# Optimization experiments

Measured on AMD Instinct MI355X. Metric: run time of the kernel, lower is better.

## Reference

```python
import jax, jax.numpy as jnp
import numpy as np

EMBED = 1024
HEADS = 16
HEAD_DIM = EMBED // HEADS


def setup_inputs() -> dict:
    key = jax.random.key(0)
    ks = jax.random.split(key, 11)
    B, S, E = 4, 2048, EMBED
    scale = 1.0 / np.sqrt(E)
    inp = {
        "Q": jax.random.normal(ks[0], (B, S, E), jnp.float32),
        "K": jax.random.normal(ks[1], (B, S, E), jnp.float32),
        "V": jax.random.normal(ks[2], (B, S, E), jnp.float32),
        "Wq": jax.random.normal(ks[3], (E, E), jnp.float32) * scale,
        "Wk": jax.random.normal(ks[4], (E, E), jnp.float32) * scale,
        "Wv": jax.random.normal(ks[5], (E, E), jnp.float32) * scale,
        "Wo": jax.random.normal(ks[6], (E, E), jnp.float32) * scale,
        "bq": jax.random.normal(ks[7], (E,), jnp.float32) * 0.01,
        "bk": jax.random.normal(ks[8], (E,), jnp.float32) * 0.01,
        "bv": jax.random.normal(ks[9], (E,), jnp.float32) * 0.01,
        "bo": jax.random.normal(ks[10], (E,), jnp.float32) * 0.01,
    }
    return inp


def reference(Q, K, V, Wq, Wk, Wv, Wo, bq, bk, bv, bo):
    B, S, E = Q.shape
    H, Dh = HEADS, HEAD_DIM
    # linear projections (torch Linear: x @ W.T + b)
    q = (Q @ Wq.T + bq).reshape(B, S, H, Dh).transpose(0, 2, 1, 3)  # [B,H,S,Dh]
    k = (K @ Wk.T + bk).reshape(B, S, H, Dh).transpose(0, 2, 1, 3)
    v = (V @ Wv.T + bv).reshape(B, S, H, Dh).transpose(0, 2, 1, 3)
    # scores [B,H,S,S]
    A = jnp.einsum('bhqd,bhkd->bhqk', q, k) / np.sqrt(Dh).astype(np.float32)
    # causal mask (mask=True)
    causal = jnp.tril(jnp.ones((S, S), dtype=bool))
    A = jnp.where(causal, A, -jnp.inf)
    w = jax.nn.softmax(A, axis=-1)
    out = jnp.einsum('bhqk,bhkd->bhqd', w, v)  # [B,H,S,Dh]
    out = out.transpose(0, 2, 1, 3).reshape(B, S, E)
    return out @ Wo.T + bo
```

## Files before the change

### kernel.cpp

```cpp
#include <hip/hip_runtime.h>
#include <hip/hip_bf16.h>
#include <hip/hip_fp16.h>

#define E_DIM 1024
#define N_HEADS 16
#define DH 64
#define BATCH 4
#define SEQ 2048
#define MROWS (BATCH * SEQ)
#define NQT 16

using half8 = __attribute__((ext_vector_type(8))) _Float16;
using half4v = __attribute__((ext_vector_type(4))) _Float16;
using fp16x2 = __attribute__((ext_vector_type(2))) __fp16;
using f32x4 = __attribute__((ext_vector_type(4))) float;

#define LOG2E 1.44269504088896340736f

__device__ inline half8 ld8(const _Float16* p) { return *(const half8*)p; }

__device__ inline uint32_t lds_off(const void* p) {
    return (uint32_t)(uintptr_t)(const __attribute__((address_space(3))) char*)p;
}

__device__ inline float exp2fast(float x) {
    float r;
    asm("v_exp_f32 %0, %1" : "=v"(r) : "v"(x));
    return r;
}

#define GLOAD_LDS(SRC, DST) \
    __builtin_amdgcn_global_load_lds( \
        (const __attribute__((address_space(1))) unsigned int*)(SRC), \
        (__attribute__((address_space(3))) unsigned int*)(DST), 16, 0, 0)

__global__ void cast4_f16(const float* __restrict__ a0, const float* __restrict__ a1,
                          const float* __restrict__ a2, const float* __restrict__ a3,
                          _Float16* __restrict__ o0, _Float16* __restrict__ o1,
                          _Float16* __restrict__ o2, _Float16* __restrict__ o3, int n4) {
    const int z = blockIdx.y;
    const float* in = z == 0 ? a0 : z == 1 ? a1 : z == 2 ? a2 : a3;
    _Float16* out = z == 0 ? o0 : z == 1 ? o1 : z == 2 ? o2 : o3;
    int i = blockIdx.x * blockDim.x + threadIdx.x;
    if (i < n4) {
        float4 v = *(const float4*)(in + (size_t)i * 4);
        half4v o;
        o[0] = (_Float16)v.x; o[1] = (_Float16)v.y;
        o[2] = (_Float16)v.z; o[3] = (_Float16)v.w;
        *(half4v*)(out + (size_t)i * 4) = o;
    }
}

template <int MODE, int AF32>
__device__ __forceinline__ void gemm_body(
    const void* __restrict__ Avoid, const _Float16* __restrict__ Bt,
    const float* __restrict__ bias, void* __restrict__ outp,
    int N, int K, float scale, char* As, _Float16* Bs)
{
    const int t = threadIdx.x;
    const int w = t >> 6, l = t & 63;
    const int wr = w >> 1, wc = w & 1;
    const int lr = l & 15, lg = l >> 4;
    const long row0 = (long)blockIdx.x * 128;
    const long col0 = (long)blockIdx.y * 128;
    f32x4 acc[4][4] = {};

    int srow[2], schk[2];
    #pragma unroll
    for (int p = 0; p < 2; ++p) {
        const int s = p * 256 + t;
        const int r0 = ((s >> 2) & 1) ^ ((s >> 4) & 1);
        srow[p] = ((s >> 3) << 1) | r0;
        schk[p] = ((s & 1) ^ r0) | (((((s >> 1) & 1) ^ ((s >> 3) & 1))) << 1);
    }

    for (int k0 = 0; k0 < K; k0 += 32) {
        __syncthreads();
        if (AF32) {
            const float* A = (const float*)Avoid;
            #pragma unroll
            for (int i = 0; i < 4; ++i) {
                const int s = i * 256 + t;
                const int row = s >> 3, c16 = (s & 7) ^ (row & 7);
                GLOAD_LDS(&A[(size_t)(row0 + row) * K + k0 + c16 * 4], As + s * 16);
            }
        } else {
            const _Float16* A = (const _Float16*)Avoid;
            #pragma unroll
            for (int p = 0; p < 2; ++p) {
                const int n = p * 256 + t;
                GLOAD_LDS(&A[(size_t)(row0 + srow[p]) * K + k0 + schk[p] * 8], As + n * 16);
            }
        }
        #pragma unroll
        for (int p = 0; p < 2; ++p) {
            const int n = p * 256 + t;
            GLOAD_LDS(&Bt[(size_t)(col0 + srow[p]) * K + k0 + schk[p] * 8], (char*)Bs + n * 16);
        }
        __syncthreads();
        half8 af[4], bf[4];
        #pragma unroll
        for (int i = 0; i < 4; i++) {
            const int row = wr * 64 + i * 16 + lr;
            if (AF32) {
                const int xr = (row & 7) << 4;
                f32x4 lo = *(const f32x4*)(As + ((row * 128 + lg * 32) ^ xr));
                f32x4 hi = *(const f32x4*)(As + ((row * 128 + lg * 32 + 16) ^ xr));
                union { fp16x2 h2[4]; half8 h8; } u;
                u.h2[0] = __builtin_amdgcn_cvt_pkrtz(lo[0], lo[1]);
                u.h2[1] = __builtin_amdgcn_cvt_pkrtz(lo[2], lo[3]);
                u.h2[2] = __builtin_amdgcn_cvt_pkrtz(hi[0], hi[1]);
                u.h2[3] = __builtin_amdgcn_cvt_pkrtz(hi[2], hi[3]);
                af[i] = u.h8;
            } else {
                af[i] = *(const half8*)(As + ((row * 64 + lg * 16) ^ ((row & 7) << 4)));
            }
            const int rowb = wc * 64 + i * 16 + lr;
            bf[i] = *(const half8*)((const char*)Bs + ((rowb * 64 + lg * 16) ^ ((rowb & 7) << 4)));
        }
        #pragma unroll
        for (int i = 0; i < 4; i++)
            #pragma unroll
            for (int j = 0; j < 4; j++)
                acc[i][j] = __builtin_amdgcn_mfma_f32_16x16x32_f16(af[i], bf[j], acc[i][j], 0, 0, 0);
    }

    #pragma unroll
    for (int i = 0; i < 4; i++)
        #pragma unroll
        for (int j = 0; j < 4; j++)
            #pragma unroll
            for (int r = 0; r < 4; r++) {
                long row = row0 + wr * 64 + i * 16 + lg * 4 + r;
                long col = col0 + wc * 64 + j * 16 + lr;
                float v = acc[i][j][r] + bias[col];
                if (MODE == 0) {
                    ((float*)outp)[row * N + col] = v;
                } else {
                    long b = row >> 11, s = row & 2047;
                    long h = col >> 6, d = col & 63;
                    ((_Float16*)outp)[(((b * N_HEADS + h) * SEQ + s) << 6) + d] =
                        (_Float16)(v * scale);
                }
            }
}

__global__ __launch_bounds__(256) void gemm_qkv(
    const float* __restrict__ A0, const float* __restrict__ A1,
    const float* __restrict__ A2,
    const _Float16* __restrict__ W0, const _Float16* __restrict__ W1,
    const _Float16* __restrict__ W2,
    const float* __restrict__ b0, const float* __restrict__ b1,
    const float* __restrict__ b2,
    _Float16* __restrict__ o0, _Float16* __restrict__ o1, _Float16* __restrict__ o2)
{
    __shared__ char As[128 * 32 * 4];
    __shared__ _Float16 Bs[128 * 32];
    const int z = blockIdx.z;
    const float* A = z == 0 ? A0 : z == 1 ? A1 : A2;
    const _Float16* W = z == 0 ? W0 : z == 1 ? W1 : W2;
    const float* bia = z == 0 ? b0 : z == 1 ? b1 : b2;
    _Float16* o = z == 0 ? o0 : z == 1 ? o1 : o2;
    const float scale = z == 0 ? (0.125f * LOG2E) : 1.0f;
    gemm_body<1, 1>(A, W, bia, o, E_DIM, E_DIM, scale, As, Bs);
}

__global__ __launch_bounds__(256) void gemm_out(
    const _Float16* __restrict__ A, const _Float16* __restrict__ W,
    const float* __restrict__ bias, float* __restrict__ o)
{
    __shared__ char As[128 * 32 * 2];
    __shared__ _Float16 Bs[128 * 32];
    gemm_body<0, 0>(A, W, bias, o, E_DIM, E_DIM, 1.0f, As, Bs);
}

__global__ __launch_bounds__(256) void attn_fwd(
    const _Float16* __restrict__ qb, const _Float16* __restrict__ kb,
    const _Float16* __restrict__ vb, _Float16* __restrict__ ob)
{
    __shared__ _Float16 sB[2 * 8192];
    const int bh = blockIdx.x;
    const int tile = (NQT - 1) - blockIdx.y;
    const int t = threadIdx.x;
    const int w = t >> 6, l = t & 63;
    const int lr = l & 15, lg = l >> 4;
    const _Float16* qh = qb + (size_t)bh * SEQ * DH;
    const char* khc = (const char*)(kb + (size_t)bh * SEQ * DH);
    const char* vhc = (const char*)(vb + (size_t)bh * SEQ * DH);
    char* sBc = (char*)sB;
    const uint32_t ldsbase = lds_off(sB);
    const int b = bh >> 4, h = bh & 15;

    int koff[2], voff[2];
    #pragma unroll
    for (int i = 0; i < 2; ++i) {
        const int s = i * 256 + t;
        { const int r = s >> 3, c = (s & 7) ^ (r & 7);
          koff[i] = r * 128 + c * 16; }
        { const int r = ((s >> 5) << 2) | ((s >> 1) & 3);
          const int c = (((s >> 3) & 3) << 1) | (s & 1);
          voff[i] = r * 128 + c * 16; }
    }

    const int nt = 2 * tile + 2;
    const int q0 = tile * 128 + w * 16;
    const int q1 = q0 + 64;

    half8 qf00 = ld8(&qh[(q0 + lr) * DH + lg * 8]);
    half8 qf01 = ld8(&qh[(q0 + lr) * DH + 32 + lg * 8]);
    half8 qf10 = ld8(&qh[(q1 + lr) * DH + lg * 8]);
    half8 qf11 = ld8(&qh[(q1 + lr) * DH + 32 + lg * 8]);

    #define STAGE(TI, BUF) do {                                                   \
        const char* ks_ = khc + (size_t)(TI) * 8192;                              \
        const char* vs_ = vhc + (size_t)(TI) * 8192;                              \
        char* kd_ = sBc + (BUF) * 16384;                                          \
        char* vd_ = kd_ + 8192;                                                   \
        _Pragma("unroll")                                                         \
        for (int i_ = 0; i_ < 2; ++i_) {                                          \
            GLOAD_LDS(ks_ + koff[i_], kd_ + i_ * 4096 + t * 16);                  \
            GLOAD_LDS(vs_ + voff[i_], vd_ + i_ * 4096 + t * 16);                  \
        }                                                                         \
    } while (0)

    STAGE(0, 0);
    STAGE(1, 1);

    f32x4 acc0[4] = {}, acc1[4] = {};
    float l0 = 0.f, l1 = 0.f;
    const f32x4 cinit = {-12.f, -12.f, -12.f, -12.f};

    int cur = 0;
    #pragma unroll 1
    for (int it = 0; it < nt; ++it) {
        if (it + 1 < nt) asm volatile("s_waitcnt vmcnt(4)" ::: "memory");
        else             asm volatile("s_waitcnt vmcnt(0)" ::: "memory");
        __builtin_amdgcn_s_barrier();

        const char* kbuf = sBc + cur * 16384;
        const uint32_t vbuf = ldsbase + (uint32_t)cur * 16384u + 8192u;
        const bool a0 = (it <= 2 * tile);
        const bool diag0 = (it == 2 * tile);
        const bool diag1 = (it == 2 * tile + 1);

        f32x4 st0[4], st1[4];
        __builtin_amdgcn_s_setprio(1);
        #pragma unroll
        for (int sub = 0; sub < 4; ++sub) {
            const int row = sub * 16 + lr;
            half8 kf0 = *(const half8*)(kbuf + ((row * 128 + lg * 16) ^ ((row & 7) << 4)));
            half8 kf1 = *(const half8*)(kbuf + ((row * 128 + 64 + lg * 16) ^ ((row & 7) << 4)));
            f32x4 s1 = __builtin_amdgcn_mfma_f32_16x16x32_f16(kf0, qf10, cinit, 0, 0, 0);
            s1 = __builtin_amdgcn_mfma_f32_16x16x32_f16(kf1, qf11, s1, 0, 0, 0);
            st1[sub] = s1;
            if (a0) {
                f32x4 s0 = __builtin_amdgcn_mfma_f32_16x16x32_f16(kf0, qf00, cinit, 0, 0, 0);
                s0 = __builtin_amdgcn_mfma_f32_16x16x32_f16(kf1, qf01, s0, 0, 0, 0);
                st0[sub] = s0;
            }
        }
        __builtin_amdgcn_s_setprio(0);

        half4v pa0[4], pa1[4];
        fp16x2 ones; ones[0] = (__fp16)1.f; ones[1] = (__fp16)1.f;

        if (a0) {
            if (diag0) {
                #pragma unroll
                for (int sub = 0; sub < 4; ++sub)
                    #pragma unroll
                    for (int r = 0; r < 4; ++r)
                        if (sub * 16 + lg * 4 + r > w * 16 + lr) st0[sub][r] = -1e30f;
            }
            float psum = 0.f;
            #pragma unroll
            for (int sub = 0; sub < 4; ++sub) {
                float pv[4];
                #pragma unroll
                for (int r = 0; r < 4; ++r) pv[r] = exp2fast(st0[sub][r]);
                fp16x2 lo = __builtin_amdgcn_cvt_pkrtz(pv[0], pv[1]);
                fp16x2 hi = __builtin_amdgcn_cvt_pkrtz(pv[2], pv[3]);
                psum = __builtin_amdgcn_fdot2(lo, ones, psum, false);
                psum = __builtin_amdgcn_fdot2(hi, ones, psum, false);
                pa0[sub][0] = (_Float16)lo[0]; pa0[sub][1] = (_Float16)lo[1];
                pa0[sub][2] = (_Float16)hi[0]; pa0[sub][3] = (_Float16)hi[1];
            }
            l0 += psum;
        }

        {
            if (diag1) {
                #pragma unroll
                for (int sub = 0; sub < 4; ++sub)
                    #pragma unroll
                    for (int r = 0; r < 4; ++r)
                        if (sub * 16 + lg * 4 + r > w * 16 + lr) st1[sub][r] = -1e30f;
            }
            float psum = 0.f;
            #pragma unroll
            for (int sub = 0; sub < 4; ++sub) {
                float pv[4];
                #pragma unroll
                for (int r = 0; r < 4; ++r) pv[r] = exp2fast(st1[sub][r]);
                fp16x2 lo = __builtin_amdgcn_cvt_pkrtz(pv[0], pv[1]);
                fp16x2 hi = __builtin_amdgcn_cvt_pkrtz(pv[2], pv[3]);
                psum = __builtin_amdgcn_fdot2(lo, ones, psum, false);
                psum = __builtin_amdgcn_fdot2(hi, ones, psum, false);
                pa1[sub][0] = (_Float16)lo[0]; pa1[sub][1] = (_Float16)lo[1];
                pa1[sub][2] = (_Float16)hi[0]; pa1[sub][3] = (_Float16)hi[1];
            }
            l1 += psum;
        }

        __builtin_amdgcn_s_setprio(1);
        #pragma unroll
        for (int sub = 0; sub < 4; ++sub) {
            const uint32_t a0addr = vbuf + (uint32_t)((sub * 4 + lg) * 512 + lr * 8);
            half4v vf0, vf1, vf2, vf3;
            asm volatile("ds_read_b64_tr_b16 %0, %1" : "=v"(vf0) : "v"(a0addr));
            asm volatile("ds_read_b64_tr_b16 %0, %1 offset:128" : "=v"(vf1) : "v"(a0addr));
            asm volatile("ds_read_b64_tr_b16 %0, %1 offset:256" : "=v"(vf2) : "v"(a0addr));
            asm volatile("ds_read_b64_tr_b16 %0, %1 offset:384" : "=v"(vf3) : "v"(a0addr));
            asm volatile("s_waitcnt lgkmcnt(0)");
            __builtin_amdgcn_sched_barrier(0);
            acc1[0] = __builtin_amdgcn_mfma_f32_16x16x16f16(pa1[sub], vf0, acc1[0], 0, 0, 0);
            acc1[1] = __builtin_amdgcn_mfma_f32_16x16x16f16(pa1[sub], vf1, acc1[1], 0, 0, 0);
            acc1[2] = __builtin_amdgcn_mfma_f32_16x16x16f16(pa1[sub], vf2, acc1[2], 0, 0, 0);
            acc1[3] = __builtin_amdgcn_mfma_f32_16x16x16f16(pa1[sub], vf3, acc1[3], 0, 0, 0);
            if (a0) {
                acc0[0] = __builtin_amdgcn_mfma_f32_16x16x16f16(pa0[sub], vf0, acc0[0], 0, 0, 0);
                acc0[1] = __builtin_amdgcn_mfma_f32_16x16x16f16(pa0[sub], vf1, acc0[1], 0, 0, 0);
                acc0[2] = __builtin_amdgcn_mfma_f32_16x16x16f16(pa0[sub], vf2, acc0[2], 0, 0, 0);
                acc0[3] = __builtin_amdgcn_mfma_f32_16x16x16f16(pa0[sub], vf3, acc0[3], 0, 0, 0);
            }
        }
        __builtin_amdgcn_s_setprio(0);

        __builtin_amdgcn_s_barrier();
        if (it + 2 < nt) STAGE(it + 2, cur);
        cur ^= 1;
    }
    #undef STAGE

    l0 += __shfl_xor(l0, 16, 64); l0 += __shfl_xor(l0, 32, 64);
    l1 += __shfl_xor(l1, 16, 64); l1 += __shfl_xor(l1, 32, 64);
    const float inv0 = 1.f / l0, inv1 = 1.f / l1;
    #pragma unroll
    for (int r = 0; r < 4; ++r) {
        const float ir0 = __shfl(inv0, lg * 4 + r, 64);
        const float ir1 = __shfl(inv1, lg * 4 + r, 64);
        const int qr0 = q0 + lg * 4 + r;
        const int qr1 = q1 + lg * 4 + r;
        #pragma unroll
        for (int db = 0; db < 4; ++db) {
            ob[((size_t)(b * SEQ + qr0)) * E_DIM + h * DH + db * 16 + lr] =
                (_Float16)(acc0[db][r] * ir0);
            ob[((size_t)(b * SEQ + qr1)) * E_DIM + h * DH + db * 16 + lr] =
                (_Float16)(acc1[db][r] * ir1);
        }
    }
}

extern "C" void kernel_launch(void* const* d_in, const int* in_sizes, int n_in,
                              void* d_out, int out_size, void* d_ws, size_t ws_size,
                              hipStream_t stream) {
    const float* Q  = (const float*)d_in[0];
    const float* K  = (const float*)d_in[1];
    const float* V  = (const float*)d_in[2];
    const float* Wq = (const float*)d_in[3];
    const float* Wk = (const float*)d_in[4];
    const float* Wv = (const float*)d_in[5];
    const float* Wo = (const float*)d_in[6];
    const float* bq = (const float*)d_in[7];
    const float* bk = (const float*)d_in[8];
    const float* bv = (const float*)d_in[9];
    const float* bo = (const float*)d_in[10];

    const size_t NX = (size_t)MROWS * E_DIM;
    const size_t NW = (size_t)E_DIM * E_DIM;

    _Float16* ws  = (_Float16*)d_ws;
    _Float16* hWq = ws;
    _Float16* hWk = hWq + NW;
    _Float16* hWv = hWk + NW;
    _Float16* hWo = hWv + NW;
    _Float16* qbf = hWo + NW;
    _Float16* kbf = qbf + NX;
    _Float16* vbf = kbf + NX;
    _Float16* aof = vbf + NX;

    const int n4w = (int)(NW / 4);
    cast4_f16<<<dim3((n4w + 255) / 256, 4), 256, 0, stream>>>(Wq, Wk, Wv, Wo, hWq, hWk, hWv, hWo, n4w);

    dim3 gg3(MROWS / 128, E_DIM / 128, 3);
    gemm_qkv<<<gg3, 256, 0, stream>>>(Q, K, V, hWq, hWk, hWv, bq, bk, bv, qbf, kbf, vbf);

    attn_fwd<<<dim3(BATCH * N_HEADS, NQT), 256, 0, stream>>>(qbf, kbf, vbf, aof);

    dim3 gg(MROWS / 128, E_DIM / 128);
    gemm_out<<<gg, 256, 0, stream>>>(aof, hWo, bo, (float*)d_out);
}
```

Before: 176.6 us.

## Software-pipeline QK^T one tile ahead and split K/V staging loads

Restructures the attention loop so the QK^T scores for the next KV tile are computed before the PV MFMAs of the current tile. This lets the softmax exponentials overlap with matrix work, and the wait only needs the K half of the next tile to have landed. Staging now issues the K loads before the V loads so that waiting with vmcnt(2) covers just K. It also adds a launch bound of 4 blocks per unit, which may cap registers and cause spills given the extra live score registers.

New measurement: 401.4 us. 127% more time.

```diff
diff --git a/kernel.cpp b/kernel.cpp
--- a/kernel.cpp
+++ b/kernel.cpp
@@ -174,7 +174,7 @@
     gemm_body<0, 0>(A, W, bias, o, E_DIM, E_DIM, 1.0f, As, Bs);
 }
 
-__global__ __launch_bounds__(256) void attn_fwd(
+__global__ __launch_bounds__(256, 4) void attn_fwd(
     const _Float16* __restrict__ qb, const _Float16* __restrict__ kb,
     const _Float16* __restrict__ vb, _Float16* __restrict__ ob)
 {
@@ -216,50 +216,54 @@
         const char* vs_ = vhc + (size_t)(TI) * 8192;                              \
         char* kd_ = sBc + (BUF) * 16384;                                          \
         char* vd_ = kd_ + 8192;                                                   \
+        GLOAD_LDS(ks_ + koff[0], kd_ + t * 16);                                   \
+        GLOAD_LDS(ks_ + koff[1], kd_ + 4096 + t * 16);                            \
+        __builtin_amdgcn_sched_barrier(0);                                        \
+        GLOAD_LDS(vs_ + voff[0], vd_ + t * 16);                                   \
+        GLOAD_LDS(vs_ + voff[1], vd_ + 4096 + t * 16);                            \
+        __builtin_amdgcn_sched_barrier(0);                                        \
+    } while (0)
+
+    #define QKT(KB, S0, S1, DO0) do {                                             \
         _Pragma("unroll")                                                         \
-        for (int i_ = 0; i_ < 2; ++i_) {                                          \
-            GLOAD_LDS(ks_ + koff[i_], kd_ + i_ * 4096 + t * 16);                  \
-            GLOAD_LDS(vs_ + voff[i_], vd_ + i_ * 4096 + t * 16);                  \
+        for (int sub = 0; sub < 4; ++sub) {                                       \
+            const int row = sub * 16 + lr;                                        \
+            half8 kf0 = *(const half8*)((KB) + ((row * 128 + lg * 16) ^ ((row & 7) << 4)));      \
+            half8 kf1 = *(const half8*)((KB) + ((row * 128 + 64 + lg * 16) ^ ((row & 7) << 4))); \
+            f32x4 s1_ = __builtin_amdgcn_mfma_f32_16x16x32_f16(kf0, qf10, cinit, 0, 0, 0); \
+            s1_ = __builtin_amdgcn_mfma_f32_16x16x32_f16(kf1, qf11, s1_, 0, 0, 0); \
+            (S1)[sub] = s1_;                                                      \
+            if (DO0) {                                                            \
+                f32x4 s0_ = __builtin_amdgcn_mfma_f32_16x16x32_f16(kf0, qf00, cinit, 0, 0, 0); \
+                s0_ = __builtin_amdgcn_mfma_f32_16x16x32_f16(kf1, qf01, s0_, 0, 0, 0); \
+                (S0)[sub] = s0_;                                                  \
+            }                                                                     \
         }                                                                         \
     } while (0)
 
+    const f32x4 cinit = {-12.f, -12.f, -12.f, -12.f};
+
     STAGE(0, 0);
     STAGE(1, 1);
 
     f32x4 acc0[4] = {}, acc1[4] = {};
     float l0 = 0.f, l1 = 0.f;
-    const f32x4 cinit = {-12.f, -12.f, -12.f, -12.f};
+
+    asm volatile("s_waitcnt vmcnt(6)" ::: "memory");
+    __builtin_amdgcn_s_barrier();
+    f32x4 st0[4], st1[4];
+    QKT(sBc, st0, st1, true);
 
     int cur = 0;
     #pragma unroll 1
     for (int it = 0; it < nt; ++it) {
-        if (it + 1 < nt) asm volatile("s_waitcnt vmcnt(4)" ::: "memory");
-        else             asm volatile("s_waitcnt vmcnt(0)" ::: "memory");
-        __builtin_amdgcn_s_barrier();
-
-        const char* kbuf = sBc + cur * 16384;
+        const char* kbufn = sBc + (cur ^ 1) * 16384;
         const uint32_t vbuf = ldsbase + (uint32_t)cur * 16384u + 8192u;
         const bool a0 = (it <= 2 * tile);
+        const bool a0n = (it + 1 <= 2 * tile);
         const bool diag0 = (it == 2 * tile);
         const bool diag1 = (it == 2 * tile + 1);
-
-        f32x4 st0[4], st1[4];
-        __builtin_amdgcn_s_setprio(1);
-        #pragma unroll
-        for (int sub = 0; sub < 4; ++sub) {
-            const int row = sub * 16 + lr;
-            half8 kf0 = *(const half8*)(kbuf + ((row * 128 + lg * 16) ^ ((row & 7) << 4)));
-            half8 kf1 = *(const half8*)(kbuf + ((row * 128 + 64 + lg * 16) ^ ((row & 7) << 4)));
-            f32x4 s1 = __builtin_amdgcn_mfma_f32_16x16x32_f16(kf0, qf10, cinit, 0, 0, 0);
-            s1 = __builtin_amdgcn_mfma_f32_16x16x32_f16(kf1, qf11, s1, 0, 0, 0);
-            st1[sub] = s1;
-            if (a0) {
-                f32x4 s0 = __builtin_amdgcn_mfma_f32_16x16x32_f16(kf0, qf00, cinit, 0, 0, 0);
-                s0 = __builtin_amdgcn_mfma_f32_16x16x32_f16(kf1, qf01, s0, 0, 0, 0);
-                st0[sub] = s0;
-            }
-        }
-        __builtin_amdgcn_s_setprio(0);
+        const bool more = (it + 1 < nt);
 
         half4v pa0[4], pa1[4];
         fp16x2 ones; ones[0] = (__fp16)1.f; ones[1] = (__fp16)1.f;
@@ -287,7 +291,6 @@
             }
             l0 += psum;
         }
-
         {
             if (diag1) {
                 #pragma unroll
@@ -311,6 +314,13 @@
             }
             l1 += psum;
         }
+
+        if (more) asm volatile("s_waitcnt vmcnt(2)" ::: "memory");
+        else      asm volatile("s_waitcnt vmcnt(0)" ::: "memory");
+        __builtin_amdgcn_s_barrier();
+
+        f32x4 st0n[4], st1n[4];
+        if (more) QKT(kbufn, st0n, st1n, a0n);
 
         __builtin_amdgcn_s_setprio(1);
         #pragma unroll
@@ -338,9 +348,15 @@
 
         __builtin_amdgcn_s_barrier();
         if (it + 2 < nt) STAGE(it + 2, cur);
+
+        if (more) {
+            #pragma unroll
+            for (int sub = 0; sub < 4; ++sub) { st0[sub] = st0n[sub]; st1[sub] = st1n[sub]; }
+        }
         cur ^= 1;
     }
     #undef STAGE
+    #undef QKT
 
     l0 += __shfl_xor(l0, 16, 64); l0 += __shfl_xor(l0, 32, 64);
     l1 += __shfl_xor(l1, 16, 64); l1 += __shfl_xor(l1, 32, 64);
```
